# Optimization experiments

Measured on AMD Instinct MI355X. Metric: run time of the kernel, lower is better.

Reference implementation:

```python
import jax, jax.numpy as jnp
import numpy as np

B, N, C, H = 2, 2048, 1024, 16
D = C // H  # head_dim = 64
EPS = 1e-6


def rmsnorm(x, w, eps=EPS):
    # RMSNorm over last dim (head_dim), matching torch RMSNorm (computed in fp32)
    x32 = x.astype(jnp.float32)
    y = x32 * jax.lax.rsqrt(jnp.mean(x32 * x32, axis=-1, keepdims=True) + eps)
    return y.astype(x.dtype) * w


def setup_inputs() -> dict:
    key = jax.random.key(0)
    ks = jax.random.split(key, 4)
    return {
        "x": jax.random.normal(ks[0], (B, N, C), dtype=jnp.float32),
        "w_qkv": jax.random.normal(ks[1], (C, 3 * C), dtype=jnp.float32) * 0.02,
        "b_qkv": jnp.zeros((3 * C,), dtype=jnp.float32),
        "q_w": jnp.ones((D,), dtype=jnp.float32),
        "k_w": jnp.ones((D,), dtype=jnp.float32),
        "w_proj": jax.random.normal(ks[2], (C, C), dtype=jnp.float32) * 0.02,
        "b_proj": jnp.zeros((C,), dtype=jnp.float32),
    }


def reference(x, w_qkv, b_qkv, q_w, k_w, w_proj, b_proj):
    b, n, c = x.shape
    h, d = H, c // H
    # QKV projection -> [3, B, H, N, D]
    qkv = (x @ w_qkv + b_qkv).reshape(b, n, 3, h, d).transpose(2, 0, 3, 1, 4)
    q, k, v = qkv[0], qkv[1], qkv[2]
    # per-head RMSNorm on q/k (qk_norm=True, use_rmsnorm=True)
    q = rmsnorm(q, q_w)
    k = rmsnorm(k, k_w)
    # scaled dot-product attention (scale = head_dim**-0.5, no dropout at eval)
    scale = d ** -0.5
    attn = jax.nn.softmax(jnp.einsum('bhqd,bhkd->bhqk', q, k) * scale, axis=-1)
    out = jnp.einsum('bhqk,bhkd->bhqd', attn, v)  # [B,H,N,D]
    out = out.transpose(0, 2, 1, 3).reshape(b, n, c)
    return out @ w_proj + b_proj
```

## Files before the change

### kernel.cpp

```cpp
#include <hip/hip_runtime.h>

typedef unsigned short u16;
typedef unsigned int u32;
typedef float f4 __attribute__((ext_vector_type(4)));
typedef __bf16 b8 __attribute__((ext_vector_type(8)));
typedef _Float16 h4 __attribute__((ext_vector_type(4)));
typedef _Float16 h8 __attribute__((ext_vector_type(8)));
typedef __fp16 hp2 __attribute__((ext_vector_type(2)));

#if __has_builtin(__builtin_amdgcn_exp2f)
#define EXP2(x) __builtin_amdgcn_exp2f(x)
#else
#define EXP2(x) exp2f(x)
#endif

__device__ __forceinline__ u16 f2bf(float f) {
  unsigned u = __float_as_uint(f);
  u += 0x7fffu + ((u >> 16) & 1u);
  return (u16)(u >> 16);
}
__device__ __forceinline__ float bf2f(u16 h) {
  return __uint_as_float(((unsigned)h) << 16);
}

__global__ void k_convert_all(const float* __restrict__ x,
                              const float* __restrict__ w_qkv,
                              const float* __restrict__ w_proj,
                              u16* __restrict__ xb, u16* __restrict__ wqkT,
                              u16* __restrict__ wpjT) {
  __shared__ u16 t[64][65];
  int bid = blockIdx.x;
  if (bid < 2048) {
    int i = (bid * 256 + threadIdx.x) * 8;
    float4 a = *(const float4*)(x + i);
    float4 b = *(const float4*)(x + i + 4);
    union { u16 h[8]; uint4 v; } r;
    r.h[0] = f2bf(a.x); r.h[1] = f2bf(a.y); r.h[2] = f2bf(a.z); r.h[3] = f2bf(a.w);
    r.h[4] = f2bf(b.x); r.h[5] = f2bf(b.y); r.h[6] = f2bf(b.z); r.h[7] = f2bf(b.w);
    *(uint4*)(xb + i) = r.v;
    return;
  }
  const float* w; u16* wT; int Ncols, Krows, bx, by;
  if (bid < 2816) { int l = bid - 2048; w = w_qkv; wT = wqkT; Ncols = 3072; Krows = 1024; bx = l % 48; by = l / 48; }
  else            { int l = bid - 2816; w = w_proj; wT = wpjT; Ncols = 1024; Krows = 1024; bx = l & 15; by = l >> 4; }
  int n0 = bx * 64, k0 = by * 64;
#pragma unroll
  for (int it = 0; it < 16; ++it) {
    int e = it * 256 + threadIdx.x;
    int r = e >> 6, c = e & 63;
    t[r][c] = f2bf(w[(size_t)(k0 + r) * Ncols + n0 + c]);
  }
  __syncthreads();
#pragma unroll
  for (int it = 0; it < 4; ++it) {
    int e = it * 256 + threadIdx.x;
    int r = e >> 4, c0 = (e & 15) * 4;
    union { u16 h[4]; uint2 v; } pk;
    pk.h[0] = t[c0][r]; pk.h[1] = t[c0 + 1][r];
    pk.h[2] = t[c0 + 2][r]; pk.h[3] = t[c0 + 3][r];
    *(uint2*)(wT + (size_t)(n0 + r) * Krows + k0 + c0) = pk.v;
  }
}

__global__ __launch_bounds__(256, 3) void k_gemm_qkv(
    const u16* __restrict__ A, const u16* __restrict__ Bt,
    const float* __restrict__ bias,
    u16* __restrict__ oq, u16* __restrict__ ok, u16* __restrict__ ov,
    const float* __restrict__ qw, const float* __restrict__ kw,
    int K) {
  __shared__ u16 lA[2][128 * 32];
  __shared__ u16 lB[2][128 * 32];
  const int tid = threadIdx.x;
  const int lane = tid & 63, lrow = lane & 15, lq = lane >> 4;
  const int wave = tid >> 6;
  const int bm = blockIdx.y * 128, bn = blockIdx.x * 128;
  const int wm = (wave >> 1) * 64, wn = (wave & 1) * 64;

  const int ch0 = tid, ch1 = 256 + tid;
  const u16* ap0 = A + (size_t)(bm + (ch0 >> 2)) * K + (ch0 & 3) * 8;
  const u16* ap1 = A + (size_t)(bm + (ch1 >> 2)) * K + (ch1 & 3) * 8;
  const u16* bp0 = Bt + (size_t)(bn + (ch0 >> 2)) * K + (ch0 & 3) * 8;
  const u16* bp1 = Bt + (size_t)(bn + (ch1 >> 2)) * K + (ch1 & 3) * 8;

  uint4 pA0 = *(const uint4*)ap0, pA1 = *(const uint4*)ap1;
  uint4 pB0 = *(const uint4*)bp0, pB1 = *(const uint4*)bp1;

  f4 acc[4][4] = {};
  const int iters = K >> 5;
  for (int it = 0; it < iters; ++it) {
    const int s = it & 1;
    *(uint4*)(lA[s] + ch0 * 8) = pA0; *(uint4*)(lA[s] + ch1 * 8) = pA1;
    *(uint4*)(lB[s] + ch0 * 8) = pB0; *(uint4*)(lB[s] + ch1 * 8) = pB1;
    if (it + 1 < iters) {
      ap0 += 32; ap1 += 32; bp0 += 32; bp1 += 32;
      pA0 = *(const uint4*)ap0; pA1 = *(const uint4*)ap1;
      pB0 = *(const uint4*)bp0; pB1 = *(const uint4*)bp1;
    }
    __syncthreads();
    b8 af[4], bf[4];
#pragma unroll
    for (int i = 0; i < 4; ++i)
      af[i] = *(const b8*)(lA[s] + (wm + i * 16 + lrow) * 32 + lq * 8);
#pragma unroll
    for (int j = 0; j < 4; ++j)
      bf[j] = *(const b8*)(lB[s] + (wn + j * 16 + lrow) * 32 + lq * 8);
#pragma unroll
    for (int i = 0; i < 4; ++i)
#pragma unroll
      for (int j = 0; j < 4; ++j)
        acc[i][j] = __builtin_amdgcn_mfma_f32_16x16x32_bf16(af[i], bf[j], acc[i][j], 0, 0, 0);
  }

  float bv[4];
#pragma unroll
  for (int j = 0; j < 4; ++j) bv[j] = bias[bn + wn + j * 16 + lrow];

  const float CS = 0.125f * 1.44269504088896340736f;
  const int n0w = bn + wn;
  const int sec = n0w >> 10;
  const int h = (n0w >> 6) & 15;
#pragma unroll
  for (int i = 0; i < 4; ++i) {
    float v[4][4];
#pragma unroll
    for (int j = 0; j < 4; ++j)
#pragma unroll
      for (int r = 0; r < 4; ++r) v[j][r] = acc[i][j][r] + bv[j];
    if (sec < 2) {
      u16* dst = sec == 0 ? oq : ok;
      const float* w = sec == 0 ? qw : kw;
      float ex = sec == 0 ? CS : 1.0f;
#pragma unroll
      for (int r = 0; r < 4; ++r) {
        float ss = v[0][r] * v[0][r] + v[1][r] * v[1][r] +
                   v[2][r] * v[2][r] + v[3][r] * v[3][r];
        ss += __shfl_xor(ss, 1, 64); ss += __shfl_xor(ss, 2, 64);
        ss += __shfl_xor(ss, 4, 64); ss += __shfl_xor(ss, 8, 64);
        float sc = rsqrtf(ss * (1.0f / 64.0f) + 1e-6f) * ex;
        int m = bm + wm + i * 16 + lq * 4 + r;
        int bb = m >> 11, ns = m & 2047;
        u16* rowp = dst + ((size_t)(bb * 16 + h) * 2048 + ns) * 64;
#pragma unroll
        for (int j = 0; j < 4; ++j) {
          int d = j * 16 + lrow;
          rowp[d] = f2bf(v[j][r] * sc * w[d]);
        }
      }
    } else {
      int m0 = bm + wm + i * 16 + lq * 4;
      int bb = m0 >> 11, ns = m0 & 2047;
#pragma unroll
      for (int j = 0; j < 4; ++j) {
        int d = j * 16 + lrow;
        union { _Float16 hh[4]; uint2 u; } pk;
#pragma unroll
        for (int r = 0; r < 4; ++r) pk.hh[r] = (_Float16)v[j][r];
        *(uint2*)(ov + ((size_t)(bb * 16 + h) * 64 + d) * 2048 + ns) = pk.u;
      }
    }
  }
}

__global__ __launch_bounds__(256, 3) void k_gemm2(
    const u16* __restrict__ A, const u16* __restrict__ Bt,
    const float* __restrict__ bias, float* __restrict__ outF,
    int K, int Ncols) {
  __shared__ u16 lA[2][128 * 32];
  __shared__ u16 lB[2][128 * 32];
  const int tid = threadIdx.x;
  const int lane = tid & 63, lrow = lane & 15, lq = lane >> 4;
  const int wave = tid >> 6;
  const int bm = blockIdx.y * 128, bn = blockIdx.x * 128;
  const int wm = (wave >> 1) * 64, wn = (wave & 1) * 64;

  const int ch0 = tid, ch1 = 256 + tid;
  const u16* ap0 = A + (size_t)(bm + (ch0 >> 2)) * K + (ch0 & 3) * 8;
  const u16* ap1 = A + (size_t)(bm + (ch1 >> 2)) * K + (ch1 & 3) * 8;
  const u16* bp0 = Bt + (size_t)(bn + (ch0 >> 2)) * K + (ch0 & 3) * 8;
  const u16* bp1 = Bt + (size_t)(bn + (ch1 >> 2)) * K + (ch1 & 3) * 8;

  uint4 pA0 = *(const uint4*)ap0, pA1 = *(const uint4*)ap1;
  uint4 pB0 = *(const uint4*)bp0, pB1 = *(const uint4*)bp1;

  f4 acc[4][4] = {};
  const int iters = K >> 5;
  for (int it = 0; it < iters; ++it) {
    const int s = it & 1;
    *(uint4*)(lA[s] + ch0 * 8) = pA0; *(uint4*)(lA[s] + ch1 * 8) = pA1;
    *(uint4*)(lB[s] + ch0 * 8) = pB0; *(uint4*)(lB[s] + ch1 * 8) = pB1;
    if (it + 1 < iters) {
      ap0 += 32; ap1 += 32; bp0 += 32; bp1 += 32;
      pA0 = *(const uint4*)ap0; pA1 = *(const uint4*)ap1;
      pB0 = *(const uint4*)bp0; pB1 = *(const uint4*)bp1;
    }
    __syncthreads();
    b8 af[4], bf[4];
#pragma unroll
    for (int i = 0; i < 4; ++i)
      af[i] = *(const b8*)(lA[s] + (wm + i * 16 + lrow) * 32 + lq * 8);
#pragma unroll
    for (int j = 0; j < 4; ++j)
      bf[j] = *(const b8*)(lB[s] + (wn + j * 16 + lrow) * 32 + lq * 8);
#pragma unroll
    for (int i = 0; i < 4; ++i)
#pragma unroll
      for (int j = 0; j < 4; ++j)
        acc[i][j] = __builtin_amdgcn_mfma_f32_16x16x32_bf16(af[i], bf[j], acc[i][j], 0, 0, 0);
  }
#pragma unroll
  for (int j = 0; j < 4; ++j) {
    int n = bn + wn + j * 16 + lrow;
    float bv = bias[n];
#pragma unroll
    for (int i = 0; i < 4; ++i)
#pragma unroll
      for (int r = 0; r < 4; ++r) {
        int m = bm + wm + i * 16 + lq * 4 + r;
        outF[(size_t)m * Ncols + n] = acc[i][j][r] + bv;
      }
  }
}

__global__ __launch_bounds__(512, 2) void k_attn(
    const u16* __restrict__ qb, const u16* __restrict__ kb,
    const u16* __restrict__ vt, u16* __restrict__ ao) {
  __shared__ u16 lK[2][128 * 72];
  __shared__ u16 lV[2][64 * 140];
  const int b = blockIdx.x;
  const int bh = b & 31;
  const int q0 = (b >> 5) * 256;
  const int tid = threadIdx.x, wave = tid >> 6, lane = tid & 63;
  const int lrow = lane & 15, lq = lane >> 4;
  const int wq = wave * 32;

  b8 qf[2][2];
#pragma unroll
  for (int g = 0; g < 2; ++g)
#pragma unroll
    for (int ks = 0; ks < 2; ++ks)
      qf[g][ks] = *(const b8*)(qb + ((size_t)bh * 2048 + q0 + wq + g * 16 + lrow) * 64 +
                               ks * 32 + lq * 8);

  f4 o[2][4] = {};
  f4 lsum[2] = {};

  const int ch0 = tid, ch1 = 512 + tid;
  const u16* kp0 = kb + (size_t)bh * 2048 * 64 + (size_t)(ch0 >> 3) * 64 + (ch0 & 7) * 8;
  const u16* kp1 = kb + (size_t)bh * 2048 * 64 + (size_t)(ch1 >> 3) * 64 + (ch1 & 7) * 8;
  const u16* vp0 = vt + (size_t)bh * 64 * 2048 + (size_t)(ch0 >> 4) * 2048 + (ch0 & 15) * 8;
  const u16* vp1 = vt + (size_t)bh * 64 * 2048 + (size_t)(ch1 >> 4) * 2048 + (ch1 & 15) * 8;
  const int kO0 = (ch0 >> 3) * 72 + (ch0 & 7) * 8;
  const int kO1 = (ch1 >> 3) * 72 + (ch1 & 7) * 8;
  const int vO0 = (ch0 >> 4) * 140 + (ch0 & 15) * 8;
  const int vO1 = (ch1 >> 4) * 140 + (ch1 & 15) * 8;

  uint4 pK0 = *(const uint4*)kp0, pK1 = *(const uint4*)kp1;
  uint4 pV0 = *(const uint4*)vp0, pV1 = *(const uint4*)vp1;

  for (int it = 0; it < 16; ++it) {
    const int s = it & 1;
    *(uint4*)(lK[s] + kO0) = pK0;
    *(uint4*)(lK[s] + kO1) = pK1;
    *(uint2*)(lV[s] + vO0) = make_uint2(pV0.x, pV0.y);
    *(uint2*)(lV[s] + vO0 + 4) = make_uint2(pV0.z, pV0.w);
    *(uint2*)(lV[s] + vO1) = make_uint2(pV1.x, pV1.y);
    *(uint2*)(lV[s] + vO1 + 4) = make_uint2(pV1.z, pV1.w);

    if (it < 15) {
      kp0 += 128 * 64; kp1 += 128 * 64; vp0 += 128; vp1 += 128;
      pK0 = *(const uint4*)kp0; pK1 = *(const uint4*)kp1;
      pV0 = *(const uint4*)vp0; pV1 = *(const uint4*)vp1;
    }
    __syncthreads();

    f4 st[2][8] = {};
#pragma unroll
    for (int ks = 0; ks < 2; ++ks)
#pragma unroll
      for (int kt = 0; kt < 8; ++kt) {
        b8 kf = *(const b8*)(lK[s] + (kt * 16 + lrow) * 72 + ks * 32 + lq * 8);
        st[0][kt] = __builtin_amdgcn_mfma_f32_16x16x32_bf16(kf, qf[0][ks], st[0][kt], 0, 0, 0);
        st[1][kt] = __builtin_amdgcn_mfma_f32_16x16x32_bf16(kf, qf[1][ks], st[1][kt], 0, 0, 0);
      }

    h8 pf[2][4];
#pragma unroll
    for (int g = 0; g < 2; ++g)
#pragma unroll
      for (int kp = 0; kp < 4; ++kp) {
        f4 eA, eB;
#pragma unroll
        for (int r = 0; r < 4; ++r) eA[r] = EXP2(st[g][2 * kp][r]);
#pragma unroll
        for (int r = 0; r < 4; ++r) eB[r] = EXP2(st[g][2 * kp + 1][r]);
        lsum[g] += eA;
        lsum[g] += eB;
        union { hp2 p2[4]; h8 v; } cv;
        cv.p2[0] = __builtin_amdgcn_cvt_pkrtz(eA[0], eA[1]);
        cv.p2[1] = __builtin_amdgcn_cvt_pkrtz(eA[2], eA[3]);
        cv.p2[2] = __builtin_amdgcn_cvt_pkrtz(eB[0], eB[1]);
        cv.p2[3] = __builtin_amdgcn_cvt_pkrtz(eB[2], eB[3]);
        pf[g][kp] = cv.v;
      }

#pragma unroll
    for (int kp = 0; kp < 4; ++kp) {
#pragma unroll
      for (int dt = 0; dt < 4; ++dt) {
        const u16* vb = lV[s] + (dt * 16 + lrow) * 140 + kp * 32 + lq * 4;
        union { h4 q[2]; h8 v; } va;
        va.q[0] = *(const h4*)vb;
        va.q[1] = *(const h4*)(vb + 16);
        o[0][dt] = __builtin_amdgcn_mfma_f32_16x16x32_f16(va.v, pf[0][kp], o[0][dt], 0, 0, 0);
        o[1][dt] = __builtin_amdgcn_mfma_f32_16x16x32_f16(va.v, pf[1][kp], o[1][dt], 0, 0, 0);
      }
    }
  }

  const int bb = bh >> 4, h = bh & 15;
#pragma unroll
  for (int g = 0; g < 2; ++g) {
    float l = lsum[g][0] + lsum[g][1] + lsum[g][2] + lsum[g][3];
    l += __shfl_xor(l, 16, 64);
    l += __shfl_xor(l, 32, 64);
    float inv = 1.0f / l;
    int q = q0 + wq + g * 16 + lrow;
#pragma unroll
    for (int dt = 0; dt < 4; ++dt) {
      union { u16 h2[4]; uint2 v; } r;
#pragma unroll
      for (int rr = 0; rr < 4; ++rr) r.h2[rr] = f2bf(o[g][dt][rr] * inv);
      *(uint2*)(ao + ((size_t)bb * 2048 + q) * 1024 + h * 64 + dt * 16 + lq * 4) = r.v;
    }
  }
}

extern "C" void kernel_launch(void* const* d_in, const int* in_sizes, int n_in,
                              void* d_out, int out_size, void* d_ws, size_t ws_size,
                              hipStream_t stream) {
  const float* x      = (const float*)d_in[0];
  const float* w_qkv  = (const float*)d_in[1];
  const float* b_qkv  = (const float*)d_in[2];
  const float* q_w    = (const float*)d_in[3];
  const float* k_w    = (const float*)d_in[4];
  const float* w_proj = (const float*)d_in[5];
  const float* b_proj = (const float*)d_in[6];
  float* out = (float*)d_out;

  u16* xb   = (u16*)d_ws;
  u16* wqkT = xb + 4194304;
  u16* wpjT = wqkT + 3145728;
  u16* qb   = wpjT + 1048576;
  u16* kb   = qb + 4194304;
  u16* vtb  = kb + 4194304;
  u16* ao   = xb;

  k_convert_all<<<3072, 256, 0, stream>>>(x, w_qkv, w_proj, xb, wqkT, wpjT);
  k_gemm_qkv<<<dim3(24, 32), 256, 0, stream>>>(xb, wqkT, b_qkv, qb, kb, vtb, q_w, k_w, 1024);
  k_attn<<<256, 512, 0, stream>>>(qb, kb, vtb, ao);
  k_gemm2<<<dim3(8, 32), 256, 0, stream>>>(ao, wpjT, b_proj, out, 1024, 1024);
}
```

Baseline: 183.1 us.

## Halve attention query tile per block, double grid, add MFMA priority hints

The attention kernel now gives each wave 16 query rows instead of 32, so each block covers 128 queries and the grid doubles to 512 blocks. Launch bounds are raised to allow 4 blocks per CU, and s_setprio brackets around the MFMA sections are meant to favour matrix issue over the exp work of other waves. The aim is better occupancy and CU coverage on a 256-CU part. In exchange, every K/V tile is loaded from global memory and written to LDS twice as often per query, which lowers reuse. LDS use per block (about 73 KB) may also cap real occupancy below the hint.

```diff
diff --git a/kernel.cpp b/kernel.cpp
--- a/kernel.cpp
+++ b/kernel.cpp
@@ -221,28 +221,26 @@
   }
 }
 
-__global__ __launch_bounds__(512, 2) void k_attn(
+__global__ __launch_bounds__(512, 4) void k_attn(
     const u16* __restrict__ qb, const u16* __restrict__ kb,
     const u16* __restrict__ vt, u16* __restrict__ ao) {
   __shared__ u16 lK[2][128 * 72];
   __shared__ u16 lV[2][64 * 140];
   const int b = blockIdx.x;
   const int bh = b & 31;
-  const int q0 = (b >> 5) * 256;
+  const int q0 = (b >> 5) * 128;
   const int tid = threadIdx.x, wave = tid >> 6, lane = tid & 63;
   const int lrow = lane & 15, lq = lane >> 4;
-  const int wq = wave * 32;
-
-  b8 qf[2][2];
-#pragma unroll
-  for (int g = 0; g < 2; ++g)
-#pragma unroll
-    for (int ks = 0; ks < 2; ++ks)
-      qf[g][ks] = *(const b8*)(qb + ((size_t)bh * 2048 + q0 + wq + g * 16 + lrow) * 64 +
-                               ks * 32 + lq * 8);
-
-  f4 o[2][4] = {};
-  f4 lsum[2] = {};
+  const int wq = wave * 16;
+
+  b8 qf[2];
+#pragma unroll
+  for (int ks = 0; ks < 2; ++ks)
+    qf[ks] = *(const b8*)(qb + ((size_t)bh * 2048 + q0 + wq + lrow) * 64 +
+                          ks * 32 + lq * 8);
+
+  f4 o[4] = {};
+  f4 lsum = {};
 
   const int ch0 = tid, ch1 = 512 + tid;
   const u16* kp0 = kb + (size_t)bh * 2048 * 64 + (size_t)(ch0 >> 3) * 64 + (ch0 & 7) * 8;
@@ -273,36 +271,36 @@
     }
     __syncthreads();
 
-    f4 st[2][8] = {};
+    f4 st[8] = {};
+    __builtin_amdgcn_s_setprio(1);
 #pragma unroll
     for (int ks = 0; ks < 2; ++ks)
 #pragma unroll
       for (int kt = 0; kt < 8; ++kt) {
         b8 kf = *(const b8*)(lK[s] + (kt * 16 + lrow) * 72 + ks * 32 + lq * 8);
-        st[0][kt] = __builtin_amdgcn_mfma_f32_16x16x32_bf16(kf, qf[0][ks], st[0][kt], 0, 0, 0);
-        st[1][kt] = __builtin_amdgcn_mfma_f32_16x16x32_bf16(kf, qf[1][ks], st[1][kt], 0, 0, 0);
-      }
-
-    h8 pf[2][4];
-#pragma unroll
-    for (int g = 0; g < 2; ++g)
-#pragma unroll
-      for (int kp = 0; kp < 4; ++kp) {
-        f4 eA, eB;
-#pragma unroll
-        for (int r = 0; r < 4; ++r) eA[r] = EXP2(st[g][2 * kp][r]);
-#pragma unroll
-        for (int r = 0; r < 4; ++r) eB[r] = EXP2(st[g][2 * kp + 1][r]);
-        lsum[g] += eA;
-        lsum[g] += eB;
-        union { hp2 p2[4]; h8 v; } cv;
-        cv.p2[0] = __builtin_amdgcn_cvt_pkrtz(eA[0], eA[1]);
-        cv.p2[1] = __builtin_amdgcn_cvt_pkrtz(eA[2], eA[3]);
-        cv.p2[2] = __builtin_amdgcn_cvt_pkrtz(eB[0], eB[1]);
-        cv.p2[3] = __builtin_amdgcn_cvt_pkrtz(eB[2], eB[3]);
-        pf[g][kp] = cv.v;
-      }
-
+        st[kt] = __builtin_amdgcn_mfma_f32_16x16x32_bf16(kf, qf[ks], st[kt], 0, 0, 0);
+      }
+    __builtin_amdgcn_s_setprio(0);
+
+    h8 pf[4];
+#pragma unroll
+    for (int kp = 0; kp < 4; ++kp) {
+      f4 eA, eB;
+#pragma unroll
+      for (int r = 0; r < 4; ++r) eA[r] = EXP2(st[2 * kp][r]);
+#pragma unroll
+      for (int r = 0; r < 4; ++r) eB[r] = EXP2(st[2 * kp + 1][r]);
+      lsum += eA;
+      lsum += eB;
+      union { hp2 p2[4]; h8 v; } cv;
+      cv.p2[0] = __builtin_amdgcn_cvt_pkrtz(eA[0], eA[1]);
+      cv.p2[1] = __builtin_amdgcn_cvt_pkrtz(eA[2], eA[3]);
+      cv.p2[2] = __builtin_amdgcn_cvt_pkrtz(eB[0], eB[1]);
+      cv.p2[3] = __builtin_amdgcn_cvt_pkrtz(eB[2], eB[3]);
+      pf[kp] = cv.v;
+    }
+
+    __builtin_amdgcn_s_setprio(1);
 #pragma unroll
     for (int kp = 0; kp < 4; ++kp) {
 #pragma unroll
@@ -311,27 +309,24 @@
         union { h4 q[2]; h8 v; } va;
         va.q[0] = *(const h4*)vb;
         va.q[1] = *(const h4*)(vb + 16);
-        o[0][dt] = __builtin_amdgcn_mfma_f32_16x16x32_f16(va.v, pf[0][kp], o[0][dt], 0, 0, 0);
-        o[1][dt] = __builtin_amdgcn_mfma_f32_16x16x32_f16(va.v, pf[1][kp], o[1][dt], 0, 0, 0);
-      }
-    }
+        o[dt] = __builtin_amdgcn_mfma_f32_16x16x32_f16(va.v, pf[kp], o[dt], 0, 0, 0);
+      }
+    }
+    __builtin_amdgcn_s_setprio(0);
   }
 
   const int bb = bh >> 4, h = bh & 15;
-#pragma unroll
-  for (int g = 0; g < 2; ++g) {
-    float l = lsum[g][0] + lsum[g][1] + lsum[g][2] + lsum[g][3];
-    l += __shfl_xor(l, 16, 64);
-    l += __shfl_xor(l, 32, 64);
-    float inv = 1.0f / l;
-    int q = q0 + wq + g * 16 + lrow;
-#pragma unroll
-    for (int dt = 0; dt < 4; ++dt) {
-      union { u16 h2[4]; uint2 v; } r;
-#pragma unroll
-      for (int rr = 0; rr < 4; ++rr) r.h2[rr] = f2bf(o[g][dt][rr] * inv);
-      *(uint2*)(ao + ((size_t)bb * 2048 + q) * 1024 + h * 64 + dt * 16 + lq * 4) = r.v;
-    }
+  float l = lsum[0] + lsum[1] + lsum[2] + lsum[3];
+  l += __shfl_xor(l, 16, 64);
+  l += __shfl_xor(l, 32, 64);
+  float inv = 1.0f / l;
+  int q = q0 + wq + lrow;
+#pragma unroll
+  for (int dt = 0; dt < 4; ++dt) {
+    union { u16 h2[4]; uint2 v; } r;
+#pragma unroll
+    for (int rr = 0; rr < 4; ++rr) r.h2[rr] = f2bf(o[dt][rr] * inv);
+    *(uint2*)(ao + ((size_t)bb * 2048 + q) * 1024 + h * 64 + dt * 16 + lq * 4) = r.v;
   }
 }
 
@@ -357,6 +352,6 @@
 
   k_convert_all<<<3072, 256, 0, stream>>>(x, w_qkv, w_proj, xb, wqkT, wpjT);
   k_gemm_qkv<<<dim3(24, 32), 256, 0, stream>>>(xb, wqkT, b_qkv, qb, kb, vtb, q_w, k_w, 1024);
-  k_attn<<<256, 512, 0, stream>>>(qb, kb, vtb, ao);
+  k_attn<<<512, 512, 0, stream>>>(qb, kb, vtb, ao);
   k_gemm2<<<dim3(8, 32), 256, 0, stream>>>(ao, wpjT, b_proj, out, 1024, 1024);
 }
```

New measurement: 187.3 us. 1.02x slower.

## Give each attention wave 64 queries and chunk the key loop to reuse K/V fragments

Applied to the files above, without the earlier changes.

The attention kernel now runs with 256 threads (4 waves) per block instead of 512, so each wave handles 64 query rows rather than 32. Each K and V fragment read from LDS is reused across four query groups, which cuts LDS traffic per MFMA. The inner loop is also split into four 32-key chunks so that fewer score registers are live at once. The trade-off is half as many waves per block, so there is less latency hiding and each thread issues twice as many global loads for the K/V tiles.

```diff
diff --git a/kernel.cpp b/kernel.cpp
--- a/kernel.cpp
+++ b/kernel.cpp
@@ -221,7 +221,7 @@
   }
 }
 
-__global__ __launch_bounds__(512, 2) void k_attn(
+__global__ __launch_bounds__(256, 1) void k_attn(
     const u16* __restrict__ qb, const u16* __restrict__ kb,
     const u16* __restrict__ vt, u16* __restrict__ ao) {
   __shared__ u16 lK[2][128 * 72];
@@ -231,68 +231,73 @@
   const int q0 = (b >> 5) * 256;
   const int tid = threadIdx.x, wave = tid >> 6, lane = tid & 63;
   const int lrow = lane & 15, lq = lane >> 4;
-  const int wq = wave * 32;
-
-  b8 qf[2][2];
-#pragma unroll
-  for (int g = 0; g < 2; ++g)
+  const int wq = wave * 64;
+
+  b8 qf[4][2];
+#pragma unroll
+  for (int g = 0; g < 4; ++g)
 #pragma unroll
     for (int ks = 0; ks < 2; ++ks)
       qf[g][ks] = *(const b8*)(qb + ((size_t)bh * 2048 + q0 + wq + g * 16 + lrow) * 64 +
                                ks * 32 + lq * 8);
 
-  f4 o[2][4] = {};
-  f4 lsum[2] = {};
-
-  const int ch0 = tid, ch1 = 512 + tid;
-  const u16* kp0 = kb + (size_t)bh * 2048 * 64 + (size_t)(ch0 >> 3) * 64 + (ch0 & 7) * 8;
-  const u16* kp1 = kb + (size_t)bh * 2048 * 64 + (size_t)(ch1 >> 3) * 64 + (ch1 & 7) * 8;
-  const u16* vp0 = vt + (size_t)bh * 64 * 2048 + (size_t)(ch0 >> 4) * 2048 + (ch0 & 15) * 8;
-  const u16* vp1 = vt + (size_t)bh * 64 * 2048 + (size_t)(ch1 >> 4) * 2048 + (ch1 & 15) * 8;
-  const int kO0 = (ch0 >> 3) * 72 + (ch0 & 7) * 8;
-  const int kO1 = (ch1 >> 3) * 72 + (ch1 & 7) * 8;
-  const int vO0 = (ch0 >> 4) * 140 + (ch0 & 15) * 8;
-  const int vO1 = (ch1 >> 4) * 140 + (ch1 & 15) * 8;
-
-  uint4 pK0 = *(const uint4*)kp0, pK1 = *(const uint4*)kp1;
-  uint4 pV0 = *(const uint4*)vp0, pV1 = *(const uint4*)vp1;
+  f4 o[4][4] = {};
+  f4 lsum[4] = {};
+
+  const u16* kbase = kb + (size_t)bh * 2048 * 64;
+  const u16* vbase = vt + (size_t)bh * 64 * 2048;
+  const u16* kp[4]; const u16* vp[4];
+  int kO[4], vO[4];
+#pragma unroll
+  for (int i = 0; i < 4; ++i) {
+    int ch = tid + 256 * i;
+    kp[i] = kbase + (size_t)(ch >> 3) * 64 + (ch & 7) * 8;
+    kO[i] = (ch >> 3) * 72 + (ch & 7) * 8;
+    vp[i] = vbase + (size_t)(ch >> 4) * 2048 + (ch & 15) * 8;
+    vO[i] = (ch >> 4) * 140 + (ch & 15) * 8;
+  }
+  uint4 pK[4], pV[4];
+#pragma unroll
+  for (int i = 0; i < 4; ++i) { pK[i] = *(const uint4*)kp[i]; pV[i] = *(const uint4*)vp[i]; }
 
   for (int it = 0; it < 16; ++it) {
     const int s = it & 1;
-    *(uint4*)(lK[s] + kO0) = pK0;
-    *(uint4*)(lK[s] + kO1) = pK1;
-    *(uint2*)(lV[s] + vO0) = make_uint2(pV0.x, pV0.y);
-    *(uint2*)(lV[s] + vO0 + 4) = make_uint2(pV0.z, pV0.w);
-    *(uint2*)(lV[s] + vO1) = make_uint2(pV1.x, pV1.y);
-    *(uint2*)(lV[s] + vO1 + 4) = make_uint2(pV1.z, pV1.w);
-
+#pragma unroll
+    for (int i = 0; i < 4; ++i) {
+      *(uint4*)(lK[s] + kO[i]) = pK[i];
+      *(uint2*)(lV[s] + vO[i]) = make_uint2(pV[i].x, pV[i].y);
+      *(uint2*)(lV[s] + vO[i] + 4) = make_uint2(pV[i].z, pV[i].w);
+    }
     if (it < 15) {
-      kp0 += 128 * 64; kp1 += 128 * 64; vp0 += 128; vp1 += 128;
-      pK0 = *(const uint4*)kp0; pK1 = *(const uint4*)kp1;
-      pV0 = *(const uint4*)vp0; pV1 = *(const uint4*)vp1;
+#pragma unroll
+      for (int i = 0; i < 4; ++i) {
+        kp[i] += 128 * 64; vp[i] += 128;
+        pK[i] = *(const uint4*)kp[i]; pV[i] = *(const uint4*)vp[i];
+      }
     }
     __syncthreads();
 
-    f4 st[2][8] = {};
-#pragma unroll
-    for (int ks = 0; ks < 2; ++ks)
-#pragma unroll
-      for (int kt = 0; kt < 8; ++kt) {
-        b8 kf = *(const b8*)(lK[s] + (kt * 16 + lrow) * 72 + ks * 32 + lq * 8);
-        st[0][kt] = __builtin_amdgcn_mfma_f32_16x16x32_bf16(kf, qf[0][ks], st[0][kt], 0, 0, 0);
-        st[1][kt] = __builtin_amdgcn_mfma_f32_16x16x32_bf16(kf, qf[1][ks], st[1][kt], 0, 0, 0);
-      }
-
-    h8 pf[2][4];
-#pragma unroll
-    for (int g = 0; g < 2; ++g)
-#pragma unroll
-      for (int kp = 0; kp < 4; ++kp) {
+#pragma unroll
+    for (int c = 0; c < 4; ++c) {
+      f4 st[4][2] = {};
+#pragma unroll
+      for (int ks = 0; ks < 2; ++ks)
+#pragma unroll
+        for (int t = 0; t < 2; ++t) {
+          b8 kf = *(const b8*)(lK[s] + ((c * 2 + t) * 16 + lrow) * 72 + ks * 32 + lq * 8);
+#pragma unroll
+          for (int g = 0; g < 4; ++g)
+            st[g][t] = __builtin_amdgcn_mfma_f32_16x16x32_bf16(kf, qf[g][ks], st[g][t], 0, 0, 0);
+        }
+
+      h8 pf[4];
+#pragma unroll
+      for (int g = 0; g < 4; ++g) {
         f4 eA, eB;
 #pragma unroll
-        for (int r = 0; r < 4; ++r) eA[r] = EXP2(st[g][2 * kp][r]);
-#pragma unroll
-        for (int r = 0; r < 4; ++r) eB[r] = EXP2(st[g][2 * kp + 1][r]);
+        for (int r = 0; r < 4; ++r) eA[r] = EXP2(st[g][0][r]);
+#pragma unroll
+        for (int r = 0; r < 4; ++r) eB[r] = EXP2(st[g][1][r]);
         lsum[g] += eA;
         lsum[g] += eB;
         union { hp2 p2[4]; h8 v; } cv;
@@ -300,26 +305,25 @@
         cv.p2[1] = __builtin_amdgcn_cvt_pkrtz(eA[2], eA[3]);
         cv.p2[2] = __builtin_amdgcn_cvt_pkrtz(eB[0], eB[1]);
         cv.p2[3] = __builtin_amdgcn_cvt_pkrtz(eB[2], eB[3]);
-        pf[g][kp] = cv.v;
-      }
-
-#pragma unroll
-    for (int kp = 0; kp < 4; ++kp) {
+        pf[g] = cv.v;
+      }
+
 #pragma unroll
       for (int dt = 0; dt < 4; ++dt) {
-        const u16* vb = lV[s] + (dt * 16 + lrow) * 140 + kp * 32 + lq * 4;
+        const u16* vb = lV[s] + (dt * 16 + lrow) * 140 + c * 32 + lq * 4;
         union { h4 q[2]; h8 v; } va;
         va.q[0] = *(const h4*)vb;
         va.q[1] = *(const h4*)(vb + 16);
-        o[0][dt] = __builtin_amdgcn_mfma_f32_16x16x32_f16(va.v, pf[0][kp], o[0][dt], 0, 0, 0);
-        o[1][dt] = __builtin_amdgcn_mfma_f32_16x16x32_f16(va.v, pf[1][kp], o[1][dt], 0, 0, 0);
+#pragma unroll
+        for (int g = 0; g < 4; ++g)
+          o[g][dt] = __builtin_amdgcn_mfma_f32_16x16x32_f16(va.v, pf[g], o[g][dt], 0, 0, 0);
       }
     }
   }
 
   const int bb = bh >> 4, h = bh & 15;
 #pragma unroll
-  for (int g = 0; g < 2; ++g) {
+  for (int g = 0; g < 4; ++g) {
     float l = lsum[g][0] + lsum[g][1] + lsum[g][2] + lsum[g][3];
     l += __shfl_xor(l, 16, 64);
     l += __shfl_xor(l, 32, 64);
@@ -357,6 +361,6 @@
 
   k_convert_all<<<3072, 256, 0, stream>>>(x, w_qkv, w_proj, xb, wqkT, wpjT);
   k_gemm_qkv<<<dim3(24, 32), 256, 0, stream>>>(xb, wqkT, b_qkv, qb, kb, vtb, q_w, k_w, 1024);
-  k_attn<<<256, 512, 0, stream>>>(qb, kb, vtb, ao);
+  k_attn<<<256, 256, 0, stream>>>(qb, kb, vtb, ao);
   k_gemm2<<<dim3(8, 32), 256, 0, stream>>>(ao, wpjT, b_proj, out, 1024, 1024);
 }
```

Result: slower. 209.8 us (+14.6%).

## Chunk attention tile into key sub-blocks and raise MFMA wave priority

Applied to the files above, without the earlier changes.

Splits each 128-key tile into four 32-key chunks, so QK^T MFMAs, exp2 softmax and PV MFMAs run per chunk instead of over the whole tile. This shrinks live score registers and lets exp work of one wave interleave with matrix work of others. It also wraps the MFMA sections in s_setprio raises to favor matrix-issuing waves. The risks are more dependency stalls inside each chunk and compiler scheduling changes.

```diff
diff --git a/kernel.cpp b/kernel.cpp
--- a/kernel.cpp
+++ b/kernel.cpp
@@ -273,26 +273,28 @@
     }
     __syncthreads();
 
-    f4 st[2][8] = {};
-#pragma unroll
-    for (int ks = 0; ks < 2; ++ks)
-#pragma unroll
-      for (int kt = 0; kt < 8; ++kt) {
-        b8 kf = *(const b8*)(lK[s] + (kt * 16 + lrow) * 72 + ks * 32 + lq * 8);
-        st[0][kt] = __builtin_amdgcn_mfma_f32_16x16x32_bf16(kf, qf[0][ks], st[0][kt], 0, 0, 0);
-        st[1][kt] = __builtin_amdgcn_mfma_f32_16x16x32_bf16(kf, qf[1][ks], st[1][kt], 0, 0, 0);
-      }
-
-    h8 pf[2][4];
-#pragma unroll
-    for (int g = 0; g < 2; ++g)
-#pragma unroll
-      for (int kp = 0; kp < 4; ++kp) {
+#pragma unroll
+    for (int c = 0; c < 4; ++c) {
+      f4 st[2][2] = {};
+      __builtin_amdgcn_s_setprio(1);
+#pragma unroll
+      for (int ks = 0; ks < 2; ++ks)
+#pragma unroll
+        for (int t = 0; t < 2; ++t) {
+          b8 kf = *(const b8*)(lK[s] + ((c * 2 + t) * 16 + lrow) * 72 + ks * 32 + lq * 8);
+          st[0][t] = __builtin_amdgcn_mfma_f32_16x16x32_bf16(kf, qf[0][ks], st[0][t], 0, 0, 0);
+          st[1][t] = __builtin_amdgcn_mfma_f32_16x16x32_bf16(kf, qf[1][ks], st[1][t], 0, 0, 0);
+        }
+      __builtin_amdgcn_s_setprio(0);
+
+      h8 pf[2];
+#pragma unroll
+      for (int g = 0; g < 2; ++g) {
         f4 eA, eB;
 #pragma unroll
-        for (int r = 0; r < 4; ++r) eA[r] = EXP2(st[g][2 * kp][r]);
-#pragma unroll
-        for (int r = 0; r < 4; ++r) eB[r] = EXP2(st[g][2 * kp + 1][r]);
+        for (int r = 0; r < 4; ++r) eA[r] = EXP2(st[g][0][r]);
+#pragma unroll
+        for (int r = 0; r < 4; ++r) eB[r] = EXP2(st[g][1][r]);
         lsum[g] += eA;
         lsum[g] += eB;
         union { hp2 p2[4]; h8 v; } cv;
@@ -300,20 +302,20 @@
         cv.p2[1] = __builtin_amdgcn_cvt_pkrtz(eA[2], eA[3]);
         cv.p2[2] = __builtin_amdgcn_cvt_pkrtz(eB[0], eB[1]);
         cv.p2[3] = __builtin_amdgcn_cvt_pkrtz(eB[2], eB[3]);
-        pf[g][kp] = cv.v;
-      }
-
-#pragma unroll
-    for (int kp = 0; kp < 4; ++kp) {
+        pf[g] = cv.v;
+      }
+
+      __builtin_amdgcn_s_setprio(1);
 #pragma unroll
       for (int dt = 0; dt < 4; ++dt) {
-        const u16* vb = lV[s] + (dt * 16 + lrow) * 140 + kp * 32 + lq * 4;
+        const u16* vb = lV[s] + (dt * 16 + lrow) * 140 + c * 32 + lq * 4;
         union { h4 q[2]; h8 v; } va;
         va.q[0] = *(const h4*)vb;
         va.q[1] = *(const h4*)(vb + 16);
-        o[0][dt] = __builtin_amdgcn_mfma_f32_16x16x32_f16(va.v, pf[0][kp], o[0][dt], 0, 0, 0);
-        o[1][dt] = __builtin_amdgcn_mfma_f32_16x16x32_f16(va.v, pf[1][kp], o[1][dt], 0, 0, 0);
-      }
+        o[0][dt] = __builtin_amdgcn_mfma_f32_16x16x32_f16(va.v, pf[0], o[0][dt], 0, 0, 0);
+        o[1][dt] = __builtin_amdgcn_mfma_f32_16x16x32_f16(va.v, pf[1], o[1][dt], 0, 0, 0);
+      }
+      __builtin_amdgcn_s_setprio(0);
     }
   }
 
```

After: 180.2 us. About the same (-1.6%).
